# Kernel tuning notes

Measured on AMD Instinct MI355X. Metric: run time of the kernel, lower is better.

## Reference

```python
import jax, jax.numpy as jnp
import numpy as np

B, T, D, H = 2, 2048, 1024, 16
DH = D // H
PD = 6
SCALE = DH ** -0.5
_PAIRS4 = [(0, 1), (0, 2), (0, 3), (1, 2), (1, 3), (2, 3)]
_J6 = jnp.array([[0, 0, 0, 0, 0, 1], [0, 0, 0, 0, -1, 0], [0, 0, 0, 1, 0, 0],
                 [0, 0, 1, 0, 0, 0], [0, -1, 0, 0, 0, 0], [1, 0, 0, 0, 0, 0]], dtype=jnp.float32)


def exterior(p1, p2):
    # p1, p2: (..., 4) -> normalized 6-d Plucker line (..., 6)
    parts = [p1[..., i] * p2[..., j] - p1[..., j] * p2[..., i] for i, j in _PAIRS4]
    L = jnp.stack(parts, axis=-1)
    n = jnp.linalg.norm(L, axis=-1, keepdims=True)
    return L / jnp.clip(n, 1e-12)


def setup_inputs() -> dict:
    key = jax.random.key(0)
    ks = jax.random.split(key, 12)
    s = 0.02
    return {
        'x': jax.random.normal(ks[0], (B, T, D), jnp.float32),
        'qkv_w': jax.random.normal(ks[1], (D, 3 * D), jnp.float32) * s,
        'qkv_b': jnp.zeros((3 * D,), jnp.float32),
        'w1_write': jax.random.normal(ks[2], (D, 4 * H), jnp.float32) * s,
        'w2_write': jax.random.normal(ks[3], (D, 4 * H), jnp.float32) * s,
        'w1_read': jax.random.normal(ks[4], (D, 4 * H), jnp.float32) * s,
        'w2_read': jax.random.normal(ks[5], (D, 4 * H), jnp.float32) * s,
        'memv_w': jax.random.normal(ks[6], (D, D), jnp.float32) * s,
        'memv_b': jnp.zeros((D,), jnp.float32),
        'memg_w': jax.random.normal(ks[7], (D, H), jnp.float32) * s,
        'memg_b': jnp.zeros((H,), jnp.float32),
        'mem_scale': jnp.full((H,), 0.1, jnp.float32),
        'rw_mix': jnp.zeros((), jnp.float32),
        'out_w': jax.random.normal(ks[8], (D, D), jnp.float32) * s,
        'out_b': jnp.zeros((D,), jnp.float32),
        'decay_logits': jnp.full((H,), 4.6, jnp.float32),
    }


def reference(x, qkv_w, qkv_b, w1_write, w2_write, w1_read, w2_read,
              memv_w, memv_b, memg_w, memg_b, mem_scale, rw_mix,
              out_w, out_b, decay_logits):
    # ---- standard causal softmax attention ----
    qkv = (x @ qkv_w + qkv_b).reshape(B, T, 3, H, DH).transpose(2, 0, 3, 1, 4)
    q, k, v = qkv[0], qkv[1], qkv[2]                      # each (B,H,T,DH)
    scores = jnp.einsum('bhtd,bhsd->bhts', q, k) * SCALE
    mask = jnp.triu(jnp.ones((T, T), bool), 1)
    scores = jnp.where(mask[None, None], -jnp.inf, scores)
    attn = jax.nn.softmax(scores, axis=-1)                # dropout=0 (eval)
    seq_out = jnp.einsum('bhts,bhsd->bthd', attn, v).reshape(B, T, D)

    # ---- Plucker lines for write (prev->cur) and read ----
    x_prev = jnp.concatenate([jnp.zeros((B, 1, D), x.dtype), x[:, :-1]], axis=1)
    w1 = (x_prev @ w1_write).reshape(B, T, H, 4)
    w2 = (x @ w2_write).reshape(B, T, H, 4)
    write_lines = exterior(w1, w2)                        # (B,T,H,6)
    r1 = (x @ w1_read).reshape(B, T, H, 4)
    r2 = (x @ w2_read).reshape(B, T, H, 4)
    read_lines = exterior(r1, r2)

    Jw = jnp.einsum('bthi,ij->bhtj', write_lines, _J6)    # (B,H,T,6)
    Jr = jnp.einsum('bthi,ij->bhtj', read_lines, _J6)
    rd = read_lines.transpose(0, 2, 1, 3)                 # (B,H,T,6)

    # ---- decay-weighted cumsum of 6x6 outer-product states ----
    decays = jax.nn.sigmoid(decay_logits)                 # (H,)
    pos = jnp.arange(T, dtype=x.dtype)
    decay_inv = (1.0 / jnp.clip(decays, 1e-6))[:, None] ** pos[None]   # (H,T)
    decay_fwd = decays[:, None] ** pos[None]                           # (H,T)

    def shifted_state(Jv):
        outer = Jv[..., :, None] * Jv[..., None, :]       # (B,H,T,6,6)
        ow = outer * decay_inv[None, :, :, None, None]
        M = jnp.cumsum(ow, axis=2)
        M = jnp.concatenate([jnp.zeros((B, H, 1, PD, PD), x.dtype), M[:, :, :-1]], axis=2)
        return M * decay_fwd[None, :, :, None, None]

    Mw = shifted_state(Jw)
    Mr = shifted_state(Jr)

    score_w = jnp.einsum('bhti,bhtij,bhtj->bht', rd, Mw, rd)
    score_r = jnp.einsum('bhti,bhtij,bhtj->bht', Jw, Mr, Jw)
    alpha = jax.nn.sigmoid(rw_mix)
    mem_score = (1 - alpha) * score_w + alpha * score_r   # (B,H,T)

    mem_val = x @ memv_w + memv_b                         # (B,T,D)
    gate = jax.nn.sigmoid(x @ memg_w + memg_b)            # (B,T,H)
    mem_score_t = mem_score.transpose(0, 2, 1)            # (B,T,H)
    gated = jax.nn.sigmoid(mem_score_t * mem_scale[None, None, :]) * gate
    gated = gated.mean(axis=-1, keepdims=True)            # (B,T,1)

    return (seq_out + gated * mem_val) @ out_w + out_b
```

## Files before the change

### kernel.cpp

```cpp
#include <hip/hip_runtime.h>

#define Bb 2
#define Tt 2048
#define Dd 1024
#define Hh 16
#define LDC 4480

typedef __attribute__((ext_vector_type(8))) short s16x8;
typedef __attribute__((ext_vector_type(4))) float f32x4;
typedef __attribute__((ext_vector_type(8))) _Float16 f16x8;

__device__ __forceinline__ float bf2f(unsigned short u) {
  unsigned v = ((unsigned)u) << 16;
  union { unsigned u; float f; } c; c.u = v; return c.f;
}
__device__ __forceinline__ unsigned short f2bf(float f) {
  union { float f; unsigned u; } c; c.f = f;
  unsigned u = c.u + 0x7fffu + ((c.u >> 16) & 1u);
  return (unsigned short)(u >> 16);
}
__device__ __forceinline__ float sigm(float x) { return 1.f / (1.f + expf(-x)); }

typedef const __attribute__((address_space(1))) void* gas_ptr;
typedef __attribute__((address_space(3))) void* las_ptr;
__device__ __forceinline__ void gload_lds16(const unsigned short* g, unsigned short* l) {
  __builtin_amdgcn_global_load_lds((gas_ptr)g, (las_ptr)l, 16, 0, 0);
}



__global__ __launch_bounds__(256) void prep_kernel(const float* __restrict__ x,
                                                   const float* __restrict__ qkv_w,
                                                   const float* __restrict__ w1w,
                                                   const float* __restrict__ w2w,
                                                   const float* __restrict__ w1r,
                                                   const float* __restrict__ w2r,
                                                   const float* __restrict__ memg_w,
                                                   const float* __restrict__ memv_w,
                                                   const float* __restrict__ out_w,
                                                   const float* __restrict__ qkv_b,
                                                   const float* __restrict__ memg_b,
                                                   const float* __restrict__ memv_b,
                                                   unsigned short* __restrict__ xb,
                                                   unsigned short* __restrict__ WT,
                                                   unsigned short* __restrict__ outT,
                                                   float* __restrict__ biasC) {
  __shared__ float tile[32][33];
  int id = blockIdx.x;
  if (id < 2048) {
    int i = id * 256 + threadIdx.x;
    int row = i >> 7;
    int k8 = i & 127;
    const float4* xv = reinterpret_cast<const float4*>(x + (size_t)i * 8);
    float4 a = xv[0], b = xv[1];
    s16x8 out;
    out[0] = (short)f2bf(a.x); out[1] = (short)f2bf(a.y);
    out[2] = (short)f2bf(a.z); out[3] = (short)f2bf(a.w);
    out[4] = (short)f2bf(b.x); out[5] = (short)f2bf(b.y);
    out[6] = (short)f2bf(b.z); out[7] = (short)f2bf(b.w);
    int mt = row >> 4, kt = k8 >> 2, quad = k8 & 3;
    int lane = (row & 15) + quad * 16;
    *(s16x8*)&xb[(((size_t)mt * 32 + kt) * 64 + lane) * 8] = out;
  } else if (id < 6528) {
    int j = id - 2048;
    int n0 = (j % 140) * 32, kt = j / 140, k0 = kt * 32;
    int tx = threadIdx.x & 31, ty = threadIdx.x >> 5;
#pragma unroll
    for (int i = 0; i < 4; i++) {
      int k = k0 + ty + i * 8, n = n0 + tx;
      float v;
      if (n < 3072)       v = qkv_w[(size_t)k * 3072 + n];
      else if (n < 3136)  v = w1w[k * 64 + (n - 3072)];
      else if (n < 3200)  v = w2w[k * 64 + (n - 3136)];
      else if (n < 3264)  v = w1r[k * 64 + (n - 3200)];
      else if (n < 3328)  v = w2r[k * 64 + (n - 3264)];
      else if (n < 3344)  v = memg_w[k * 16 + (n - 3328)];
      else if (n < 3392)  v = 0.f;
      else if (n < 4416)  v = memv_w[(size_t)k * 1024 + (n - 3392)];
      else                v = 0.f;
      tile[ty + i * 8][tx] = v;
    }
    __syncthreads();
    if (threadIdx.x < 128) {
      int nl = threadIdx.x & 31, quad = threadIdx.x >> 5;
      s16x8 out;
#pragma unroll
      for (int e = 0; e < 8; e++) out[e] = (short)f2bf(tile[quad * 8 + e][nl]);
      int nt = (n0 >> 4) + (nl >> 4);
      int lane = (nl & 15) + quad * 16;
      *(s16x8*)&WT[(((size_t)nt * 32 + kt) * 64 + lane) * 8] = out;
    }
  } else if (id < 7552) {
    int j = id - 6528;
    int n0 = (j & 31) * 32, kt = j >> 5, k0 = kt * 32;
    int tx = threadIdx.x & 31, ty = threadIdx.x >> 5;
#pragma unroll
    for (int i = 0; i < 4; i++) {
      int k = k0 + ty + i * 8, n = n0 + tx;
      tile[ty + i * 8][tx] = out_w[(size_t)k * 1024 + n];
    }
    __syncthreads();
    if (threadIdx.x < 128) {
      int nl = threadIdx.x & 31, quad = threadIdx.x >> 5;
      s16x8 out;
#pragma unroll
      for (int e = 0; e < 8; e++) out[e] = (short)f2bf(tile[quad * 8 + e][nl]);
      int nt = (n0 >> 4) + (nl >> 4);
      int lane = (nl & 15) + quad * 16;
      *(s16x8*)&outT[(((size_t)nt * 32 + kt) * 64 + lane) * 8] = out;
    }
  } else {
    int i = (id - 7552) * 256 + threadIdx.x;
    if (i < LDC) {
      float v = 0.f;
      if (i < 3072) v = qkv_b[i];
      else if (i >= 3328 && i < 3344) v = memg_b[i - 3328];
      else if (i >= 3392 && i < 4416) v = memv_b[i - 3392];
      biasC[i] = v;
    }
  }
}


template <int MODE>
__global__ __launch_bounds__(256) void gemm_frag_kernel(const unsigned short* __restrict__ Af,
                                                        const unsigned short* __restrict__ Bf,
                                                        void* __restrict__ Cout,
                                                        const float* __restrict__ bias) {
  __shared__ __align__(16) unsigned short lds[2][16][512];
  int mTile, nTile;
  if (MODE == 0) {
    const int xx = blockIdx.x & 7, local = blockIdx.x >> 3;
    mTile = (xx >> 1) * 8 + (local & 7);
    nTile = (xx & 1) * 18 + (local >> 3);
    if (nTile >= 35) return;
  } else {
    mTile = blockIdx.x >> 3;
    nTile = blockIdx.x & 7;
  }
  const int lane = threadIdx.x & 63, wid = threadIdx.x >> 6;
  const int quad = lane >> 4, c16 = lane & 15;
  const int wm = wid >> 1, wn = wid & 1;
  const int mt0 = mTile * 8 + wm * 4;
  const int nt0 = nTile * 8 + wn * 4;

  const unsigned short* src[4];
#pragma unroll
  for (int i = 0; i < 4; i++) {
    int f = wid * 4 + i;
    src[i] = ((f < 8) ? (Af + (size_t)(mTile * 8 + f) * 16384)
                      : (Bf + (size_t)(nTile * 8 + (f - 8)) * 16384))
             + (size_t)lane * 8;
  }

  f32x4 acc[4][4] = {};

#pragma unroll
  for (int i = 0; i < 4; i++) gload_lds16(src[i], &lds[0][wid * 4 + i][0]);
  __syncthreads();

  int buf = 0;
  for (int kt = 0; kt < 32; kt++) {
    if (kt + 1 < 32) {
#pragma unroll
      for (int i = 0; i < 4; i++)
        gload_lds16(src[i] + (size_t)(kt + 1) * 512, &lds[buf ^ 1][wid * 4 + i][0]);
    }
    s16x8 a[4], b[4];
#pragma unroll
    for (int i = 0; i < 4; i++) {
      a[i] = *(const s16x8*)&lds[buf][wm * 4 + i][lane * 8];
      b[i] = *(const s16x8*)&lds[buf][8 + wn * 4 + i][lane * 8];
    }
#pragma unroll
    for (int mt = 0; mt < 4; mt++)
#pragma unroll
      for (int nt = 0; nt < 4; nt++)
        acc[mt][nt] = __builtin_amdgcn_mfma_f32_16x16x32_bf16(a[mt], b[nt],
                                                              acc[mt][nt], 0, 0, 0);
    __syncthreads();
    buf ^= 1;
  }

#pragma unroll
  for (int mt = 0; mt < 4; mt++)
#pragma unroll
    for (int nt = 0; nt < 4; nt++) {
      int col = (nt0 + nt) * 16 + c16;
      float bv = bias[col];
#pragma unroll
      for (int r = 0; r < 4; r++) {
        int row = (mt0 + mt) * 16 + quad * 4 + r;
        if (MODE == 0)
          ((unsigned short*)Cout)[(size_t)row * 4480 + col] = f2bf(acc[mt][nt][r] + bv);
        else
          ((float*)Cout)[(size_t)row * 1024 + col] = acc[mt][nt][r] + bv;
      }
    }
}


__device__ __forceinline__ void ext6(const float* p, const float* q, float* L) {
  L[0] = p[0] * q[1] - p[1] * q[0];
  L[1] = p[0] * q[2] - p[2] * q[0];
  L[2] = p[0] * q[3] - p[3] * q[0];
  L[3] = p[1] * q[2] - p[2] * q[1];
  L[4] = p[1] * q[3] - p[3] * q[1];
  L[5] = p[2] * q[3] - p[3] * q[2];
  float n = sqrtf(L[0]*L[0] + L[1]*L[1] + L[2]*L[2] + L[3]*L[3] + L[4]*L[4] + L[5]*L[5]);
  float inv = 1.f / fmaxf(n, 1e-12f);
#pragma unroll
  for (int k = 0; k < 6; k++) L[k] *= inv;
}


__global__ __launch_bounds__(256) void post1_kernel(const unsigned short* __restrict__ Cq,
                                                    unsigned short* __restrict__ Kt,
                                                    unsigned short* __restrict__ Vt,
                                                    float* __restrict__ Jw,
                                                    float* __restrict__ Jr,
                                                    float* __restrict__ rd) {
  __shared__ unsigned short vt[32 * 66];
  int id = blockIdx.x;
  int tid = threadIdx.x;
  if (id < 2048) {
    int kb = id & 63, bh = id >> 6;
    int b = bh >> 4, h = bh & 15;
    size_t tbase = ((size_t)bh * 64 + kb) * 2048;
    {
      int key = tid >> 3, p = tid & 7, dg = p ^ (key & 7);
      size_t src = (size_t)(b * Tt + kb * 32 + key) * LDC + 1024 + h * 64 + dg * 8;
      s16x8 kv = *(const s16x8*)&Cq[src];
      s16x8 kvs;
#pragma unroll
      for (int e = 0; e < 8; e++)
        kvs[e] = (short)f2bf(bf2f((unsigned short)kv[e]) * 0.125f);
      *(s16x8*)&Kt[tbase + (size_t)tid * 8] = kvs;
    }
    {
      int row = tid >> 3, c = tid & 7;
      size_t src = (size_t)(b * Tt + kb * 32 + row) * LDC + 2048 + h * 64 + c * 8;
      s16x8 vv = *(const s16x8*)&Cq[src];
#pragma unroll
      for (int e = 0; e < 8; e++) {
        union { _Float16 hf; unsigned short s; } cv;
        cv.hf = (_Float16)bf2f((unsigned short)vv[e]);
        vt[row * 66 + c * 8 + e] = cv.s;
      }
    }
    __syncthreads();
    {
      int d = tid >> 2, p = tid & 3, cq = p ^ ((d >> 2) & 3);
      s16x8 out;
#pragma unroll
      for (int e = 0; e < 8; e++) {
        int key = ((e >> 2) & 1) * 16 + cq * 4 + (e & 3);
        out[e] = (short)vt[key * 66 + d];
      }
      *(s16x8*)&Vt[tbase + (size_t)tid * 8] = out;
    }
  } else {
    int idx = (id - 2048) * 256 + tid;
    int h = idx & 15, t = (idx >> 4) & 2047, b = idx >> 15;
    size_t row = (size_t)(b * Tt + t) * LDC;
    float w1[4], w2[4], r1[4], r2[4];
#pragma unroll
    for (int k = 0; k < 4; k++) {
      w1[k] = (t > 0) ? bf2f(Cq[row - LDC + 3072 + h * 4 + k]) : 0.f;
      w2[k] = bf2f(Cq[row + 3136 + h * 4 + k]);
      r1[k] = bf2f(Cq[row + 3200 + h * 4 + k]);
      r2[k] = bf2f(Cq[row + 3264 + h * 4 + k]);
    }
    float Lw[6], Lr[6];
    ext6(w1, w2, Lw);
    ext6(r1, r2, Lr);
    size_t ob = ((size_t)(b * Hh + h) * Tt + t) * 6;
    Jw[ob + 0] = Lw[5]; Jw[ob + 1] = -Lw[4]; Jw[ob + 2] = Lw[3];
    Jw[ob + 3] = Lw[2]; Jw[ob + 4] = -Lw[1]; Jw[ob + 5] = Lw[0];
    Jr[ob + 0] = Lr[5]; Jr[ob + 1] = -Lr[4]; Jr[ob + 2] = Lr[3];
    Jr[ob + 3] = Lr[2]; Jr[ob + 4] = -Lr[1]; Jr[ob + 5] = Lr[0];
#pragma unroll
    for (int k = 0; k < 6; k++) rd[ob + k] = Lr[k];
  }
}


__device__ __forceinline__ void do_tile(int ks, int q0, int quad, int c16,
                                        const s16x8& qf0, const s16x8& qf1,
                                        const s16x8 kf[2][2], const f16x8 vb[4],
                                        float& l_i, f32x4 o[4]) {
  f32x4 st0 = {}, st1 = {};
  __builtin_amdgcn_s_setprio(1);
  st0 = __builtin_amdgcn_mfma_f32_16x16x32_bf16(kf[0][0], qf0, st0, 0, 0, 0);
  st0 = __builtin_amdgcn_mfma_f32_16x16x32_bf16(kf[0][1], qf1, st0, 0, 0, 0);
  st1 = __builtin_amdgcn_mfma_f32_16x16x32_bf16(kf[1][0], qf0, st1, 0, 0, 0);
  st1 = __builtin_amdgcn_mfma_f32_16x16x32_bf16(kf[1][1], qf1, st1, 0, 0, 0);
  __builtin_amdgcn_s_setprio(0);
  bool need_mask = (ks + 31 > q0);
  f16x8 pa;
  float lp = 0.f;
#pragma unroll
  for (int r = 0; r < 4; r++) {
    float v0 = st0[r];
    float v1 = st1[r];
    if (need_mask) {
      v0 = (ks + quad * 4 + r      <= q0 + c16) ? v0 : -1e30f;
      v1 = (ks + 16 + quad * 4 + r <= q0 + c16) ? v1 : -1e30f;
    }
    float p0 = __expf(v0);
    float p1 = __expf(v1);
    lp += p0 + p1;
    pa[r]     = (_Float16)p0;
    pa[4 + r] = (_Float16)p1;
  }
  l_i += lp;
  __builtin_amdgcn_s_setprio(1);
#pragma unroll
  for (int nt = 0; nt < 4; nt++)
    o[nt] = __builtin_amdgcn_mfma_f32_16x16x32_f16(pa, vb[nt], o[nt], 0, 0, 0);
  __builtin_amdgcn_s_setprio(0);
}

__global__ __launch_bounds__(128) void attn_kernel(const unsigned short* __restrict__ Cq,
                                                   const unsigned short* __restrict__ Kt,
                                                   const unsigned short* __restrict__ Vt,
                                                   unsigned short* __restrict__ po) {
  __shared__ float mrg[64][35];
  const int id = blockIdx.x;
  const int xcd = id & 7, rest = id >> 3;
  const int pi = rest & 63;
  const int bh = ((rest >> 6) << 3) | xcd;
  const int b = bh >> 4, h = bh & 15;
  const int kw = threadIdx.x >> 6, lane = threadIdx.x & 63;
  const int quad = lane >> 4, c16 = lane & 15;
  const int qA = pi * 16, qB = 2032 - pi * 16;
  const int nkA = qA + 16, nkB = 2048 - pi * 16;
  const int TA = (nkA + 31) >> 5, TB = (nkB + 31) >> 5;
  const int ht = (TA >= 16) ? 16 : (32 - TA);
  const int t0 = kw ? ht : 0;
  const int t1 = kw ? TB : ht;
  const char* Kbase = (const char*)(Kt + (size_t)bh * 64 * 2048);
  const char* Vbase = (const char*)(Vt + (size_t)bh * 64 * 2048);
  const int vK0 = c16 * 128 + ((quad       ^ (c16 & 7)) * 16);
  const int vK1 = c16 * 128 + (((4 + quad) ^ (c16 & 7)) * 16);
  const int vV  = c16 * 64  + ((quad ^ ((c16 >> 2) & 3)) * 16);

  size_t rowA = (size_t)(b * Tt + qA + c16) * LDC + h * 64;
  size_t rowB = (size_t)(b * Tt + qB + c16) * LDC + h * 64;
  s16x8 qA0 = *(const s16x8*)&Cq[rowA + quad * 8];
  s16x8 qA1 = *(const s16x8*)&Cq[rowA + 32 + quad * 8];
  s16x8 qB0 = *(const s16x8*)&Cq[rowB + quad * 8];
  s16x8 qB1 = *(const s16x8*)&Cq[rowB + 32 + quad * 8];

  float lA = 0.f, lB = 0.f;
  f32x4 oA[4] = {}, oB[4] = {};

  s16x8 kfX[2][2], kfY[2][2];
  f16x8 vbX[4], vbY[4];

#define LOADT(dstK, dstV, kb) do {                                   \
    const char* Kb_ = Kbase + (size_t)(kb) * 4096;                   \
    const char* Vb_ = Vbase + (size_t)(kb) * 4096;                   \
    dstK[0][0] = *(const s16x8*)(Kb_ + vK0);                         \
    dstK[0][1] = *(const s16x8*)(Kb_ + vK1);                         \
    dstK[1][0] = *(const s16x8*)(Kb_ + 2048 + vK0);                  \
    dstK[1][1] = *(const s16x8*)(Kb_ + 2048 + vK1);                  \
    dstV[0] = *(const f16x8*)(Vb_ + vV);                             \
    dstV[1] = *(const f16x8*)(Vb_ + 1024 + vV);                      \
    dstV[2] = *(const f16x8*)(Vb_ + 2048 + vV);                      \
    dstV[3] = *(const f16x8*)(Vb_ + 3072 + vV);                      \
  } while (0)

  LOADT(kfX, vbX, t0);
  for (int t = t0; t < t1; t += 2) {
    if (t + 1 < t1) LOADT(kfY, vbY, t + 1);
    {
      int ks = t * 32;
      do_tile(ks, qB, quad, c16, qB0, qB1, kfX, vbX, lB, oB);
      if (ks < nkA)
        do_tile(ks, qA, quad, c16, qA0, qA1, kfX, vbX, lA, oA);
    }
    if (t + 1 < t1) {
      if (t + 2 < t1) LOADT(kfX, vbX, t + 2);
      int ks = (t + 1) * 32;
      do_tile(ks, qB, quad, c16, qB0, qB1, kfY, vbY, lB, oB);
      if (ks < nkA)
        do_tile(ks, qA, quad, c16, qA0, qA1, kfY, vbY, lA, oA);
    }
  }
#undef LOADT

  if (kw == 1) {
#pragma unroll
    for (int nt = 0; nt < 4; nt++)
#pragma unroll
      for (int r = 0; r < 4; r++) {
        mrg[lane][nt * 4 + r]      = oB[nt][r];
        mrg[lane][16 + nt * 4 + r] = oA[nt][r];
      }
    mrg[lane][32] = lB;
    mrg[lane][33] = lA;
  }
  __syncthreads();
  if (kw == 1) return;
#pragma unroll
  for (int nt = 0; nt < 4; nt++)
#pragma unroll
    for (int r = 0; r < 4; r++) {
      oB[nt][r] += mrg[lane][nt * 4 + r];
      oA[nt][r] += mrg[lane][16 + nt * 4 + r];
    }
  lB += mrg[lane][32];
  lA += mrg[lane][33];

  lB += __shfl_xor(lB, 16, 64); lB += __shfl_xor(lB, 32, 64);
  lA += __shfl_xor(lA, 16, 64); lA += __shfl_xor(lA, 32, 64);
  float invB = 1.f / lB, invA = 1.f / lA;
#pragma unroll
  for (int r = 0; r < 4; r++) {
    float ivB = __shfl(invB, quad * 4 + r, 64);
    float ivA = __shfl(invA, quad * 4 + r, 64);
    size_t baseB = (size_t)(b * Tt + qB + quad * 4 + r) * Dd + h * 64;
    size_t baseA = (size_t)(b * Tt + qA + quad * 4 + r) * Dd + h * 64;
#pragma unroll
    for (int nt = 0; nt < 4; nt++) {
      po[baseB + nt * 16 + c16] = f2bf(oB[nt][r] * ivB);
      po[baseA + nt * 16 + c16] = f2bf(oA[nt][r] * ivA);
    }
  }
}


__global__ __launch_bounds__(64) void scanA_kernel(const float* __restrict__ Jw,
                                                   const float* __restrict__ Jr,
                                                   const float* __restrict__ decay_logits,
                                                   float* __restrict__ chunkA) {
  int blk = blockIdx.x;
  int chunk = blk & 15, bh = (blk >> 4) & 31, type = blk >> 9;
  int lane = threadIdx.x;
  const float* V = (type == 0 ? Jw : Jr) + ((size_t)bh * Tt + chunk * 128) * 6;
  __shared__ float v[768];
  for (int i = lane; i < 768; i += 64) v[i] = V[i];
  __syncthreads();
  float d = sigm(decay_logits[bh & 15]);
  int ll = lane < 36 ? lane : 35;
  int i6 = ll / 6, j6 = ll % 6;
  float A = 0.f;
  for (int s = 0; s < 128; s++) A = d * A + v[s * 6 + i6] * v[s * 6 + j6];
  if (lane < 36) chunkA[((size_t)(type * 32 + bh) * 16 + chunk) * 36 + lane] = A;
}


__global__ __launch_bounds__(128) void scanB_kernel(const float* __restrict__ Jw,
                                                    const float* __restrict__ Jr,
                                                    const float* __restrict__ rd,
                                                    const float* __restrict__ chunkA,
                                                    const float* __restrict__ decay_logits,
                                                    float* __restrict__ score_w,
                                                    float* __restrict__ score_r) {
  int blk = blockIdx.x;
  int chunk = blk & 15, bh = (blk >> 4) & 31, type = blk >> 9;
  int tl = threadIdx.x;
  size_t tb = ((size_t)bh * Tt + chunk * 128) * 6;
  const float* U = (type == 0 ? rd : Jw) + tb;
  const float* W = (type == 0 ? Jw : Jr) + tb;
  __shared__ float wv[768];
  __shared__ float Bm[36];
  for (int i = tl; i < 768; i += 128) wv[i] = W[i];
  float d = sigm(decay_logits[bh & 15]);
  if (tl < 36) {
    float dS = powf(d, 128.f);
    float Bv = 0.f;
    size_t base = (size_t)(type * 32 + bh) * 16;
    for (int c = 0; c < chunk; c++)
      Bv = dS * Bv + d * chunkA[(base + c) * 36 + tl];
    Bm[tl] = Bv;
  }
  __syncthreads();
  float u[6];
#pragma unroll
  for (int i = 0; i < 6; i++) u[i] = U[tl * 6 + i];
  float q = 0.f;
#pragma unroll
  for (int i = 0; i < 6; i++) {
    float bi = 0.f;
#pragma unroll
    for (int j = 0; j < 6; j++) bi += Bm[i * 6 + j] * u[j];
    q += u[i] * bi;
  }
  float acc = 0.f;
  for (int s = 0; s < tl; s++) {
    const float* ws = &wv[s * 6];
    float dot = u[0]*ws[0] + u[1]*ws[1] + u[2]*ws[2] + u[3]*ws[3] + u[4]*ws[4] + u[5]*ws[5];
    acc = d * (acc + dot * dot);
  }
  float score = acc + powf(d, (float)tl) * q;
  float* outp = (type == 0 ? score_w : score_r);
  outp[(size_t)bh * Tt + chunk * 128 + tl] = score;
}


__global__ __launch_bounds__(256) void combine_kernel(const unsigned short* __restrict__ po,
                                                      const unsigned short* __restrict__ Cq,
                                                      const float* __restrict__ score_w,
                                                      const float* __restrict__ score_r,
                                                      const float* __restrict__ mem_scale,
                                                      const float* __restrict__ rw_mix,
                                                      unsigned short* __restrict__ fused) {
  __shared__ float tmp[16];
  int rowi = blockIdx.x;
  int b = rowi >> 11, t = rowi & 2047;
  float alpha = sigm(rw_mix[0]);
  if (threadIdx.x < 16) {
    int h = threadIdx.x;
    size_t sh = (size_t)(b * 16 + h) * Tt + t;
    float ms = (1.f - alpha) * score_w[sh] + alpha * score_r[sh];
    float gate = sigm(bf2f(Cq[(size_t)rowi * LDC + 3328 + h]));
    tmp[h] = sigm(ms * mem_scale[h]) * gate;
  }
  __syncthreads();
  float g = 0.f;
#pragma unroll
  for (int h = 0; h < 16; h++) g += tmp[h];
  g *= (1.f / 16.f);
  if (threadIdx.x < 128) {
    int c = threadIdx.x;
    int d0 = c * 8;
    s16x8 ov = *(const s16x8*)&po[((size_t)b * Tt + t) * Dd + d0];
    s16x8 mv = *(const s16x8*)&Cq[(size_t)rowi * LDC + 3392 + d0];
    s16x8 out;
#pragma unroll
    for (int e = 0; e < 8; e++)
      out[e] = (short)f2bf(bf2f((unsigned short)ov[e]) + g * bf2f((unsigned short)mv[e]));
    int mt = rowi >> 4, kt = c >> 2, quad = c & 3;
    int lane = (rowi & 15) + quad * 16;
    *(s16x8*)&fused[(((size_t)mt * 32 + kt) * 64 + lane) * 8] = out;
  }
}


extern "C" void kernel_launch(void* const* d_in, const int* in_sizes, int n_in,
                              void* d_out, int out_size, void* d_ws, size_t ws_size,
                              hipStream_t stream) {
  (void)in_sizes; (void)n_in; (void)out_size; (void)ws_size;
  const float* x         = (const float*)d_in[0];
  const float* qkv_w     = (const float*)d_in[1];
  const float* qkv_b     = (const float*)d_in[2];
  const float* w1w       = (const float*)d_in[3];
  const float* w2w       = (const float*)d_in[4];
  const float* w1r       = (const float*)d_in[5];
  const float* w2r       = (const float*)d_in[6];
  const float* memv_w    = (const float*)d_in[7];
  const float* memv_b    = (const float*)d_in[8];
  const float* memg_w    = (const float*)d_in[9];
  const float* memg_b    = (const float*)d_in[10];
  const float* mem_scale = (const float*)d_in[11];
  const float* rw_mix    = (const float*)d_in[12];
  const float* out_w     = (const float*)d_in[13];
  const float* out_b     = (const float*)d_in[14];
  const float* decay_l   = (const float*)d_in[15];

  char* w = (char*)d_ws;
  unsigned short* xb    = (unsigned short*)(w + 0);
  unsigned short* Kt    = (unsigned short*)(w + 0);
  unsigned short* WT    = (unsigned short*)(w + 8388608);
  unsigned short* Vt    = (unsigned short*)(w + 8388608);
  unsigned short* outT  = (unsigned short*)(w + 17563648);
  float*          biasC = (float*)(w + 19660800);
  unsigned short* Cbuf  = (unsigned short*)(w + 19678720);
  unsigned short* po    = (unsigned short*)(w + 56378880);
  float*          Jw    = (float*)(w + 73680384);
  float*          Jr    = (float*)(w + 75253248);
  float*          rd    = (float*)(w + 76826112);
  float*          chA   = (float*)(w + 78398976);
  float*          sw    = (float*)(w + 78693888);
  float*          sr    = (float*)(w + 78956032);
  unsigned short* fused = (unsigned short*)(w + 79218176);

  prep_kernel<<<7570, 256, 0, stream>>>(x, qkv_w, w1w, w2w, w1r, w2r, memg_w, memv_w,
                                        out_w, qkv_b, memg_b, memv_b,
                                        xb, WT, outT, biasC);

  gemm_frag_kernel<0><<<1152, 256, 0, stream>>>(xb, WT, Cbuf, biasC);

  post1_kernel<<<2304, 256, 0, stream>>>(Cbuf, Kt, Vt, Jw, Jr, rd);
  attn_kernel<<<2048, 128, 0, stream>>>(Cbuf, Kt, Vt, po);
  scanA_kernel<<<1024, 64, 0, stream>>>(Jw, Jr, decay_l, chA);
  scanB_kernel<<<1024, 128, 0, stream>>>(Jw, Jr, rd, chA, decay_l, sw, sr);
  combine_kernel<<<4096, 256, 0, stream>>>(po, Cbuf, sw, sr, mem_scale, rw_mix, fused);

  gemm_frag_kernel<1><<<256, 256, 0, stream>>>(fused, outT, d_out, out_b);
}
```

Measured before the change: 281.5 us.

## Process four 16-row query tiles per attention block to reuse K/V loads

Each attention block now handles two adjacent 16-row query tiles from the front and two from the back of the sequence, instead of one of each, and the grid is halved. Every K/V tile loaded into registers feeds up to four do_tile calls, so K/V global traffic and load instructions per unit of work drop by about half. In exchange the kernel holds twice as many Q fragments and output accumulators, which raises register pressure, so launch_bounds now requests 2 blocks per SIMD/CU. The LDS merge buffer is enlarged to match. The smaller grid with longer blocks may also leave the GPU less evenly loaded.

```diff
diff --git a/kernel.cpp b/kernel.cpp
--- a/kernel.cpp
+++ b/kernel.cpp
@@ -321,39 +321,45 @@
   __builtin_amdgcn_s_setprio(0);
 }
 
-__global__ __launch_bounds__(128) void attn_kernel(const unsigned short* __restrict__ Cq,
-                                                   const unsigned short* __restrict__ Kt,
-                                                   const unsigned short* __restrict__ Vt,
-                                                   unsigned short* __restrict__ po) {
-  __shared__ float mrg[64][35];
+__global__ __launch_bounds__(128, 2) void attn_kernel(const unsigned short* __restrict__ Cq,
+                                                      const unsigned short* __restrict__ Kt,
+                                                      const unsigned short* __restrict__ Vt,
+                                                      unsigned short* __restrict__ po) {
+  __shared__ float mrg[64][69];
   const int id = blockIdx.x;
   const int xcd = id & 7, rest = id >> 3;
-  const int pi = rest & 63;
-  const int bh = ((rest >> 6) << 3) | xcd;
+  const int j = rest & 31;
+  const int bh = ((rest >> 5) << 3) | xcd;
   const int b = bh >> 4, h = bh & 15;
   const int kw = threadIdx.x >> 6, lane = threadIdx.x & 63;
   const int quad = lane >> 4, c16 = lane & 15;
-  const int qA = pi * 16, qB = 2032 - pi * 16;
-  const int nkA = qA + 16, nkB = 2048 - pi * 16;
-  const int TA = (nkA + 31) >> 5, TB = (nkB + 31) >> 5;
-  const int ht = (TA >= 16) ? 16 : (32 - TA);
+  const int qA0r = j * 32,        qA1r = j * 32 + 16;
+  const int qB0r = 2016 - j * 32, qB1r = 2032 - j * 32;
+  const int Ttot = 64 - j;
+  const int ht = (j >= 16) ? 16 : (32 - j);
   const int t0 = kw ? ht : 0;
-  const int t1 = kw ? TB : ht;
+  const int t1 = kw ? Ttot : ht;
   const char* Kbase = (const char*)(Kt + (size_t)bh * 64 * 2048);
   const char* Vbase = (const char*)(Vt + (size_t)bh * 64 * 2048);
   const int vK0 = c16 * 128 + ((quad       ^ (c16 & 7)) * 16);
   const int vK1 = c16 * 128 + (((4 + quad) ^ (c16 & 7)) * 16);
   const int vV  = c16 * 64  + ((quad ^ ((c16 >> 2) & 3)) * 16);
 
-  size_t rowA = (size_t)(b * Tt + qA + c16) * LDC + h * 64;
-  size_t rowB = (size_t)(b * Tt + qB + c16) * LDC + h * 64;
-  s16x8 qA0 = *(const s16x8*)&Cq[rowA + quad * 8];
-  s16x8 qA1 = *(const s16x8*)&Cq[rowA + 32 + quad * 8];
-  s16x8 qB0 = *(const s16x8*)&Cq[rowB + quad * 8];
-  s16x8 qB1 = *(const s16x8*)&Cq[rowB + 32 + quad * 8];
-
-  float lA = 0.f, lB = 0.f;
-  f32x4 oA[4] = {}, oB[4] = {};
+  size_t rowA0 = (size_t)(b * Tt + qA0r + c16) * LDC + h * 64;
+  size_t rowA1 = (size_t)(b * Tt + qA1r + c16) * LDC + h * 64;
+  size_t rowB0 = (size_t)(b * Tt + qB0r + c16) * LDC + h * 64;
+  size_t rowB1 = (size_t)(b * Tt + qB1r + c16) * LDC + h * 64;
+  s16x8 qa00 = *(const s16x8*)&Cq[rowA0 + quad * 8];
+  s16x8 qa01 = *(const s16x8*)&Cq[rowA0 + 32 + quad * 8];
+  s16x8 qa10 = *(const s16x8*)&Cq[rowA1 + quad * 8];
+  s16x8 qa11 = *(const s16x8*)&Cq[rowA1 + 32 + quad * 8];
+  s16x8 qb00 = *(const s16x8*)&Cq[rowB0 + quad * 8];
+  s16x8 qb01 = *(const s16x8*)&Cq[rowB0 + 32 + quad * 8];
+  s16x8 qb10 = *(const s16x8*)&Cq[rowB1 + quad * 8];
+  s16x8 qb11 = *(const s16x8*)&Cq[rowB1 + 32 + quad * 8];
+
+  float lA0 = 0.f, lA1 = 0.f, lB0 = 0.f, lB1 = 0.f;
+  f32x4 oA0[4] = {}, oA1[4] = {}, oB0[4] = {}, oB1[4] = {};
 
   s16x8 kfX[2][2], kfY[2][2];
   f16x8 vbX[4], vbY[4];
@@ -371,23 +377,26 @@
     dstV[3] = *(const f16x8*)(Vb_ + 3072 + vV);                      \
   } while (0)
 
+#define DOTILES(KF, VF, t) do {                                      \
+    int ks_ = (t) * 32;                                              \
+    do_tile(ks_, qB0r, quad, c16, qb00, qb01, KF, VF, lB0, oB0);     \
+    do_tile(ks_, qB1r, quad, c16, qb10, qb11, KF, VF, lB1, oB1);     \
+    if ((t) <= j) {                                                  \
+      do_tile(ks_, qA0r, quad, c16, qa00, qa01, KF, VF, lA0, oA0);   \
+      do_tile(ks_, qA1r, quad, c16, qa10, qa11, KF, VF, lA1, oA1);   \
+    }                                                                \
+  } while (0)
+
   LOADT(kfX, vbX, t0);
   for (int t = t0; t < t1; t += 2) {
     if (t + 1 < t1) LOADT(kfY, vbY, t + 1);
-    {
-      int ks = t * 32;
-      do_tile(ks, qB, quad, c16, qB0, qB1, kfX, vbX, lB, oB);
-      if (ks < nkA)
-        do_tile(ks, qA, quad, c16, qA0, qA1, kfX, vbX, lA, oA);
-    }
+    DOTILES(kfX, vbX, t);
     if (t + 1 < t1) {
       if (t + 2 < t1) LOADT(kfX, vbX, t + 2);
-      int ks = (t + 1) * 32;
-      do_tile(ks, qB, quad, c16, qB0, qB1, kfY, vbY, lB, oB);
-      if (ks < nkA)
-        do_tile(ks, qA, quad, c16, qA0, qA1, kfY, vbY, lA, oA);
-    }
-  }
+      DOTILES(kfY, vbY, t + 1);
+    }
+  }
+#undef DOTILES
 #undef LOADT
 
   if (kw == 1) {
@@ -395,11 +404,15 @@
     for (int nt = 0; nt < 4; nt++)
 #pragma unroll
       for (int r = 0; r < 4; r++) {
-        mrg[lane][nt * 4 + r]      = oB[nt][r];
-        mrg[lane][16 + nt * 4 + r] = oA[nt][r];
+        mrg[lane][nt * 4 + r]      = oB0[nt][r];
+        mrg[lane][16 + nt * 4 + r] = oB1[nt][r];
+        mrg[lane][32 + nt * 4 + r] = oA0[nt][r];
+        mrg[lane][48 + nt * 4 + r] = oA1[nt][r];
       }
-    mrg[lane][32] = lB;
-    mrg[lane][33] = lA;
+    mrg[lane][64] = lB0;
+    mrg[lane][65] = lB1;
+    mrg[lane][66] = lA0;
+    mrg[lane][67] = lA1;
   }
   __syncthreads();
   if (kw == 1) return;
@@ -407,25 +420,38 @@
   for (int nt = 0; nt < 4; nt++)
 #pragma unroll
     for (int r = 0; r < 4; r++) {
-      oB[nt][r] += mrg[lane][nt * 4 + r];
-      oA[nt][r] += mrg[lane][16 + nt * 4 + r];
-    }
-  lB += mrg[lane][32];
-  lA += mrg[lane][33];
-
-  lB += __shfl_xor(lB, 16, 64); lB += __shfl_xor(lB, 32, 64);
-  lA += __shfl_xor(lA, 16, 64); lA += __shfl_xor(lA, 32, 64);
-  float invB = 1.f / lB, invA = 1.f / lA;
+      oB0[nt][r] += mrg[lane][nt * 4 + r];
+      oB1[nt][r] += mrg[lane][16 + nt * 4 + r];
+      oA0[nt][r] += mrg[lane][32 + nt * 4 + r];
+      oA1[nt][r] += mrg[lane][48 + nt * 4 + r];
+    }
+  lB0 += mrg[lane][64];
+  lB1 += mrg[lane][65];
+  lA0 += mrg[lane][66];
+  lA1 += mrg[lane][67];
+
+  lB0 += __shfl_xor(lB0, 16, 64); lB0 += __shfl_xor(lB0, 32, 64);
+  lB1 += __shfl_xor(lB1, 16, 64); lB1 += __shfl_xor(lB1, 32, 64);
+  lA0 += __shfl_xor(lA0, 16, 64); lA0 += __shfl_xor(lA0, 32, 64);
+  lA1 += __shfl_xor(lA1, 16, 64); lA1 += __shfl_xor(lA1, 32, 64);
+  float invB0 = 1.f / lB0, invB1 = 1.f / lB1;
+  float invA0 = 1.f / lA0, invA1 = 1.f / lA1;
 #pragma unroll
   for (int r = 0; r < 4; r++) {
-    float ivB = __shfl(invB, quad * 4 + r, 64);
-    float ivA = __shfl(invA, quad * 4 + r, 64);
-    size_t baseB = (size_t)(b * Tt + qB + quad * 4 + r) * Dd + h * 64;
-    size_t baseA = (size_t)(b * Tt + qA + quad * 4 + r) * Dd + h * 64;
+    float ivB0 = __shfl(invB0, quad * 4 + r, 64);
+    float ivB1 = __shfl(invB1, quad * 4 + r, 64);
+    float ivA0 = __shfl(invA0, quad * 4 + r, 64);
+    float ivA1 = __shfl(invA1, quad * 4 + r, 64);
+    size_t bB0 = (size_t)(b * Tt + qB0r + quad * 4 + r) * Dd + h * 64;
+    size_t bB1 = (size_t)(b * Tt + qB1r + quad * 4 + r) * Dd + h * 64;
+    size_t bA0 = (size_t)(b * Tt + qA0r + quad * 4 + r) * Dd + h * 64;
+    size_t bA1 = (size_t)(b * Tt + qA1r + quad * 4 + r) * Dd + h * 64;
 #pragma unroll
     for (int nt = 0; nt < 4; nt++) {
-      po[baseB + nt * 16 + c16] = f2bf(oB[nt][r] * ivB);
-      po[baseA + nt * 16 + c16] = f2bf(oA[nt][r] * ivA);
+      po[bB0 + nt * 16 + c16] = f2bf(oB0[nt][r] * ivB0);
+      po[bB1 + nt * 16 + c16] = f2bf(oB1[nt][r] * ivB1);
+      po[bA0 + nt * 16 + c16] = f2bf(oA0[nt][r] * ivA0);
+      po[bA1 + nt * 16 + c16] = f2bf(oA1[nt][r] * ivA1);
     }
   }
 }
@@ -584,7 +610,7 @@
   gemm_frag_kernel<0><<<1152, 256, 0, stream>>>(xb, WT, Cbuf, biasC);
 
   post1_kernel<<<2304, 256, 0, stream>>>(Cbuf, Kt, Vt, Jw, Jr, rd);
-  attn_kernel<<<2048, 128, 0, stream>>>(Cbuf, Kt, Vt, po);
+  attn_kernel<<<1024, 128, 0, stream>>>(Cbuf, Kt, Vt, po);
   scanA_kernel<<<1024, 64, 0, stream>>>(Jw, Jr, decay_l, chA);
   scanB_kernel<<<1024, 128, 0, stream>>>(Jw, Jr, rd, chA, decay_l, sw, sr);
   combine_kernel<<<4096, 256, 0, stream>>>(po, Cbuf, sw, sr, mem_scale, rw_mix, fused);
```

Result: faster. 253.5 us, median of 2 (-9.9%).
